# Kernel optimization log

Measured on AMD Instinct MI355X. Metric: run time of the kernel, lower is better.

The kernel has to match this reference:

```python
import jax, jax.numpy as jnp
import numpy as np

EPS = 1e-10


def setup_inputs() -> dict:
    key = jax.random.key(0)
    k1, k2, k3 = jax.random.split(key, 3)
    B, T, N = 32, 512, 128
    transition = jax.random.uniform(k1, (N, N), dtype=jnp.float32)
    log_emission = jax.random.normal(k2, (B, T, N), dtype=jnp.float32)
    prior = jax.random.uniform(k3, (N,), dtype=jnp.float32)
    return {"transition": transition, "log_emission": log_emission, "prior": prior}


def reference(transition, log_emission, prior):
    B, T, N = log_emission.shape
    # clamp + row-normalize transition (matches torch: clamp, clamp/sum(dim=1))
    trans = jnp.clip(transition, EPS)
    trans = jnp.clip(trans, EPS) / jnp.sum(trans, axis=1, keepdims=True)
    log_trans_T = jnp.log(trans).T  # (N, N): [next, prev]

    pr = jnp.clip(prior, EPS)
    pr = pr / jnp.sum(pr)
    log_prior = jnp.log(pr)

    # initial trellis row
    log0 = log_prior[None, :] + log_emission[:, 0]  # (B, N)
    em_rest = jnp.transpose(log_emission[:, 1:], (1, 0, 2))  # (T-1, B, N)

    def fwd_step(prev_log, em_t):
        # scores[b, next, prev] = prev_log[b, prev] + log_trans_T[next, prev]
        scores = prev_log[:, None, :] + log_trans_T[None, :, :]  # (B, N, N)
        m = jnp.max(scores, axis=-1, keepdims=True)
        e = jnp.exp(scores - m)
        Z = jnp.sum(e, axis=-1, keepdims=True)
        soft_max = jnp.squeeze(jnp.log(Z) + m, -1)  # logsumexp, (B, N)
        new_log = em_t + soft_max
        bp = e / Z  # soft backpointers, (B, N, N)
        return new_log, bp

    last_log, bps = jax.lax.scan(fwd_step, log0, em_rest)  # bps: (T-1, B, N, N)

    final_probs = jax.nn.softmax(last_log, axis=1)  # (B, N)

    def bwd_step(p_next, bp_t):
        # soft_path[t] = soft_path[t+1] @ bp[t]
        p = jnp.einsum("bn,bnm->bm", p_next, bp_t)
        return p, p

    _, path_prefix = jax.lax.scan(bwd_step, final_probs, bps, reverse=True)  # (T-1, B, N)

    soft_path = jnp.concatenate([path_prefix, final_probs[None]], axis=0)  # (T, B, N)
    return jnp.transpose(soft_path, (1, 0, 2))  # (B, T, N)
```

## Files before the change

### kernel.cpp

```cpp
#include <hip/hip_runtime.h>
#include <math.h>


#define TT 512
#define BB 32
#define NN 128
#define EPSC 1e-10f
#define TINY 1e-33f

#define BAR() asm volatile("s_waitcnt lgkmcnt(0)\n\ts_barrier" ::: "memory")

__device__ __forceinline__ float qswap1(float x) {
  return __int_as_float(__builtin_amdgcn_mov_dpp(__float_as_int(x), 0xB1, 0xF, 0xF, true));
}
__device__ __forceinline__ float qswap2(float x) {
  return __int_as_float(__builtin_amdgcn_mov_dpp(__float_as_int(x), 0x4E, 0xF, 0xF, true));
}

__device__ __forceinline__ void dot32(const float4 av[8], const float tm[2][32], float z[2]) {
  #pragma unroll
  for (int s = 0; s < 2; ++s) {
    float a0 = 0.f, a1 = 0.f, a2 = 0.f, a3 = 0.f;
    #pragma unroll
    for (int i = 0; i < 8; ++i) {
      a0 = fmaf(av[i].x, tm[s][4*i+0], a0);
      a1 = fmaf(av[i].y, tm[s][4*i+1], a1);
      a2 = fmaf(av[i].z, tm[s][4*i+2], a2);
      a3 = fmaf(av[i].w, tm[s][4*i+3], a3);
    }
    float zz = (a0 + a1) + (a2 + a3);
    zz += qswap1(zz);
    zz += qswap2(zz);
    z[s] = zz;
  }
}

__global__ __launch_bounds__(256, 1)
void soft_viterbi_kernel(const float* __restrict__ trans,
                         const float* __restrict__ emis,
                         const float* __restrict__ prior,
                         float* __restrict__ out) {
  const int b    = blockIdx.x;
  const int tid  = threadIdx.x;
  const int w    = tid >> 6;
  const int lane = tid & 63;
  const int k    = lane & 3;
  const int pid  = lane >> 2;
  const int n0   = 32 * w + 2 * pid;

  __shared__ __align__(16) float ubuf[2][NN];
  __shared__ __align__(16) float sarr[TT];
  __shared__ __align__(16) float red[NN];

  const float* embq = emis + (size_t)b * TT * NN + n0;
  float* outb = out + (size_t)b * TT * NN;

  float2 pr2 = *(const float2*)(prior + n0);
  float2 em0 = *(const float2*)(embq);
  float2 e1  = *(const float2*)(embq + 1 * NN);
  float2 e2  = *(const float2*)(embq + 2 * NN);
  float2 e3  = *(const float2*)(embq + 3 * NN);
  pr2.x = fmaxf(pr2.x, EPSC); pr2.y = fmaxf(pr2.y, EPSC);

  if (tid < NN) {
    const float4* row = (const float4*)(trans + tid * NN);
    float s = 0.f;
    #pragma unroll 8
    for (int j = 0; j < NN / 4; ++j) {
      float4 v = row[j];
      s += fmaxf(v.x, EPSC) + fmaxf(v.y, EPSC) + fmaxf(v.z, EPSC) + fmaxf(v.w, EPSC);
    }
    red[tid] = s;
  }
  __syncthreads();

  float tf[2][32];
  #pragma unroll
  for (int i = 0; i < 8; ++i) {
    #pragma unroll
    for (int c = 0; c < 4; ++c) {
      const int p = 4 * (k + 4 * i) + c;
      const float2 tv = *(const float2*)(trans + p * NN + n0);
      const float rp = red[p];
      tf[0][4*i+c] = fmaxf(tv.x, EPSC) / rp;
      tf[1][4*i+c] = fmaxf(tv.y, EPSC) / rp;
    }
  }
  float tb[2][32];
  #pragma unroll
  for (int s = 0; s < 2; ++s) {
    const float inv = 1.0f / red[n0 + s];
    const float4* rr = (const float4*)(trans + (n0 + s) * NN);
    #pragma unroll
    for (int i = 0; i < 8; ++i) {
      const float4 tv = rr[k + 4 * i];
      tb[s][4*i+0] = fmaxf(tv.x, EPSC) * inv;
      tb[s][4*i+1] = fmaxf(tv.y, EPSC) * inv;
      tb[s][4*i+2] = fmaxf(tv.z, EPSC) * inv;
      tb[s][4*i+3] = fmaxf(tv.w, EPSC) * inv;
    }
  }

  float vv = (k == 0) ? (pr2.x + pr2.y) : 0.f;
  #pragma unroll
  for (int m = 1; m < 64; m <<= 1) vv += __shfl_xor(vv, m, 64);
  __syncthreads();
  if (lane == 0) red[w] = vv;
  __syncthreads();
  const float psum = (red[0] + red[1]) + (red[2] + red[3]);

  float an0 = (pr2.x / psum) * __expf(em0.x);
  float an1 = (pr2.y / psum) * __expf(em0.y);
  if (k == 0) {
    float2 a2 = make_float2(an0, an1);
    *(float2*)&ubuf[0][n0] = a2;
    *(float2*)(outb + n0) = a2;
  }
  float dc0 = __expf(e1.x), dc1 = __expf(e1.y);
  float2 eh1 = e2;
  float2 eh2 = e3;
  float dl0 = dc0, dl1 = dc1;
  BAR();

  for (int t = 1; t < TT; ++t) {
    const float* rb = ubuf[(t - 1) & 1];
    const float r0 = rb[0];
    const float4* rb4 = (const float4*)rb;
    float4 av[8];
    #pragma unroll
    for (int i = 0; i < 8; ++i) av[i] = rb4[k + 4 * i];
    float z[2];
    dot32(av, tf, z);
    const float rinv = 1.0f / r0;
    dl0 = dc0; dl1 = dc1;
    an0 = (dc0 * rinv) * z[0];
    an1 = (dc1 * rinv) * z[1];
    dc0 = __expf(eh1.x); dc1 = __expf(eh1.y);
    eh1 = eh2;
    const int tpre = (t + 3 < TT) ? (t + 3) : (TT - 1);
    eh2 = *(const float2*)(embq + (size_t)tpre * NN);
    if (k == 0) {
      float2 a2 = make_float2(an0, an1);
      *(float2*)&ubuf[t & 1][n0] = a2;
      if (t < TT - 1) *(float2*)(outb + (size_t)t * NN + n0) = a2;
    }
    if (tid == 0) sarr[t - 1] = rinv;
    BAR();
  }

  float v2 = (k == 0) ? (an0 + an1) : 0.f;
  #pragma unroll
  for (int m = 1; m < 64; m <<= 1) v2 += __shfl_xor(v2, m, 64);
  if (lane == 0) red[w] = v2;
  __syncthreads();
  const float total = (red[0] + red[1]) + (red[2] + red[3]);
  const float itot = 1.0f / total;
  float pc0 = an0 * itot, pc1 = an1 * itot;
  if (k == 0) *(float2*)(outb + (size_t)(TT - 1) * NN + n0) = make_float2(pc0, pc1);

  asm volatile("s_waitcnt vmcnt(0)" ::: "memory");

  float2 ec_cur = *(const float2*)(outb + (size_t)(TT - 2) * NN + n0);
  float2 ec_h   = *(const float2*)(outb + (size_t)(TT - 3) * NN + n0);
  float2 em_b1  = *(const float2*)(embq + (size_t)(TT - 2) * NN);
  float2 em_b2  = *(const float2*)(embq + (size_t)(TT - 3) * NN);
  const float sl = sarr[TT - 2];
  float g0 = dl0 * sl / fmaxf(an0, TINY);
  float g1 = dl1 * sl / fmaxf(an1, TINY);

  for (int t = TT - 2; t >= 0; --t) {
    if (k == 0) {
      *(float2*)&ubuf[t & 1][n0] = make_float2(pc0 * g0, pc1 * g1);
    }
    const float sr = sarr[(t > 0) ? (t - 1) : 0];
    const float gn0 = __expf(em_b1.x) * sr / fmaxf(ec_cur.x, TINY);
    const float gn1 = __expf(em_b1.y) * sr / fmaxf(ec_cur.y, TINY);
    em_b1 = em_b2;
    const int tp = (t >= 2) ? (t - 2) : 0;
    em_b2 = *(const float2*)(embq + (size_t)tp * NN);
    BAR();
    const float4* qb4 = (const float4*)ubuf[t & 1];
    float4 av[8];
    #pragma unroll
    for (int i = 0; i < 8; ++i) av[i] = qb4[k + 4 * i];
    float z[2];
    dot32(av, tb, z);
    pc0 = ec_cur.x * z[0];
    pc1 = ec_cur.y * z[1];
    if (k == 0) *(float2*)(outb + (size_t)t * NN + n0) = make_float2(pc0, pc1);
    g0 = gn0; g1 = gn1;
    ec_cur = ec_h;
    ec_h = *(const float2*)(outb + (size_t)tp * NN + n0);
  }
}

extern "C" void kernel_launch(void* const* d_in, const int* in_sizes, int n_in,
                              void* d_out, int out_size, void* d_ws, size_t ws_size,
                              hipStream_t stream) {
  (void)in_sizes; (void)n_in; (void)d_ws; (void)ws_size; (void)out_size;
  const float* trans = (const float*)d_in[0];
  const float* emis  = (const float*)d_in[1];
  const float* prior = (const float*)d_in[2];
  float* out = (float*)d_out;
  soft_viterbi_kernel<<<dim3(BB), dim3(256), 0, stream>>>(trans, emis, prior, out);
}
```

Before: 452.3 us.

## Collapse per-batch block to a single wavefront, removing barriers from recurrence

Each batch sequence now runs on one 64-lane wavefront instead of four. The forward and backward recurrences can then drop s_barrier entirely and use a single LDS buffer with only compiler fences. Each lane now computes 8 output dot products with packed float2 FMAs and selects its two outputs after DPP reductions. Division is also replaced by hardware reciprocal. The cost is 4x more FLOPs per lane, very heavy register use (two 128-float transition tiles), and possible LDS ordering hazards that now rely on in-wave execution order.

Measured after the change: 901.0 us. +99.2%, slower.

```diff
diff --git a/kernel.cpp b/kernel.cpp
--- a/kernel.cpp
+++ b/kernel.cpp
@@ -8,8 +8,13 @@
 #define EPSC 1e-10f
 #define TINY 1e-33f
 
-#define BAR() asm volatile("s_waitcnt lgkmcnt(0)\n\ts_barrier" ::: "memory")
-
+typedef float v2f __attribute__((ext_vector_type(2)));
+
+#define CFENCE() asm volatile("" ::: "memory")
+
+__device__ __forceinline__ float rcp_fast(float x) {
+  return __builtin_amdgcn_rcpf(x);
+}
 __device__ __forceinline__ float qswap1(float x) {
   return __int_as_float(__builtin_amdgcn_mov_dpp(__float_as_int(x), 0xB1, 0xF, 0xF, true));
 }
@@ -17,180 +22,187 @@
   return __int_as_float(__builtin_amdgcn_mov_dpp(__float_as_int(x), 0x4E, 0xF, 0xF, true));
 }
 
-__device__ __forceinline__ void dot32(const float4 av[8], const float tm[2][32], float z[2]) {
-  #pragma unroll
-  for (int s = 0; s < 2; ++s) {
-    float a0 = 0.f, a1 = 0.f, a2 = 0.f, a3 = 0.f;
-    #pragma unroll
-    for (int i = 0; i < 8; ++i) {
-      a0 = fmaf(av[i].x, tm[s][4*i+0], a0);
-      a1 = fmaf(av[i].y, tm[s][4*i+1], a1);
-      a2 = fmaf(av[i].z, tm[s][4*i+2], a2);
-      a3 = fmaf(av[i].w, tm[s][4*i+3], a3);
-    }
-    float zz = (a0 + a1) + (a2 + a3);
-    zz += qswap1(zz);
-    zz += qswap2(zz);
-    z[s] = zz;
-  }
-}
-
-__global__ __launch_bounds__(256, 1)
+__device__ __forceinline__ float dot16pk(const v2f* av, const v2f* tm) {
+  v2f a0 = av[0] * tm[0];
+  v2f a1 = av[1] * tm[1];
+  #pragma unroll
+  for (int j = 2; j < 16; j += 2) {
+    a0 = __builtin_elementwise_fma(av[j+0], tm[j+0], a0);
+    a1 = __builtin_elementwise_fma(av[j+1], tm[j+1], a1);
+  }
+  v2f s = a0 + a1;
+  return s.x + s.y;
+}
+
+__global__ __launch_bounds__(64, 1)
 void soft_viterbi_kernel(const float* __restrict__ trans,
                          const float* __restrict__ emis,
                          const float* __restrict__ prior,
                          float* __restrict__ out) {
   const int b    = blockIdx.x;
-  const int tid  = threadIdx.x;
-  const int w    = tid >> 6;
-  const int lane = tid & 63;
+  const int lane = threadIdx.x;
+  const int g    = lane >> 2;
   const int k    = lane & 3;
-  const int pid  = lane >> 2;
-  const int n0   = 32 * w + 2 * pid;
-
-  __shared__ __align__(16) float ubuf[2][NN];
+  const int s0   = 8 * g + 2 * k;
+  const int nf0  = 8 * g;
+  const bool k1  = (k & 1) != 0;
+  const bool k2  = (k & 2) != 0;
+
+  __shared__ __align__(16) float ubuf[NN];
   __shared__ __align__(16) float sarr[TT];
   __shared__ __align__(16) float red[NN];
 
-  const float* embq = emis + (size_t)b * TT * NN + n0;
-  float* outb = out + (size_t)b * TT * NN;
-
-  float2 pr2 = *(const float2*)(prior + n0);
-  float2 em0 = *(const float2*)(embq);
-  float2 e1  = *(const float2*)(embq + 1 * NN);
-  float2 e2  = *(const float2*)(embq + 2 * NN);
-  float2 e3  = *(const float2*)(embq + 3 * NN);
+  const float* emB = emis + (size_t)b * TT * NN;
+  float* outb      = out  + (size_t)b * TT * NN;
+
+  float2 pr2 = *(const float2*)(prior + s0);
+  float2 em0 = *(const float2*)(emB + s0);
+  float2 e1  = *(const float2*)(emB + 1 * NN + s0);
+  float2 e2  = *(const float2*)(emB + 2 * NN + s0);
+  float2 e3  = *(const float2*)(emB + 3 * NN + s0);
   pr2.x = fmaxf(pr2.x, EPSC); pr2.y = fmaxf(pr2.y, EPSC);
 
-  if (tid < NN) {
-    const float4* row = (const float4*)(trans + tid * NN);
+  #pragma unroll
+  for (int rr = 0; rr < 2; ++rr) {
+    const int r = 2 * lane + rr;
+    const float4* row = (const float4*)(trans + r * NN);
     float s = 0.f;
     #pragma unroll 8
     for (int j = 0; j < NN / 4; ++j) {
       float4 v = row[j];
       s += fmaxf(v.x, EPSC) + fmaxf(v.y, EPSC) + fmaxf(v.z, EPSC) + fmaxf(v.w, EPSC);
     }
-    red[tid] = s;
-  }
-  __syncthreads();
-
-  float tf[2][32];
+    red[r] = s;
+  }
+  CFENCE();
+
+  v2f tf[8][16];
   #pragma unroll
   for (int i = 0; i < 8; ++i) {
     #pragma unroll
     for (int c = 0; c < 4; ++c) {
       const int p = 4 * (k + 4 * i) + c;
-      const float2 tv = *(const float2*)(trans + p * NN + n0);
-      const float rp = red[p];
-      tf[0][4*i+c] = fmaxf(tv.x, EPSC) / rp;
-      tf[1][4*i+c] = fmaxf(tv.y, EPSC) / rp;
+      const float4 ta = *(const float4*)(trans + p * NN + nf0);
+      const float4 tc = *(const float4*)(trans + p * NN + nf0 + 4);
+      const float ir = 1.0f / red[p];
+      const int jj = 2 * i + (c >> 1); const int ee = c & 1;
+      tf[0][jj][ee] = fmaxf(ta.x, EPSC) * ir;
+      tf[1][jj][ee] = fmaxf(ta.y, EPSC) * ir;
+      tf[2][jj][ee] = fmaxf(ta.z, EPSC) * ir;
+      tf[3][jj][ee] = fmaxf(ta.w, EPSC) * ir;
+      tf[4][jj][ee] = fmaxf(tc.x, EPSC) * ir;
+      tf[5][jj][ee] = fmaxf(tc.y, EPSC) * ir;
+      tf[6][jj][ee] = fmaxf(tc.z, EPSC) * ir;
+      tf[7][jj][ee] = fmaxf(tc.w, EPSC) * ir;
     }
   }
-  float tb[2][32];
-  #pragma unroll
-  for (int s = 0; s < 2; ++s) {
-    const float inv = 1.0f / red[n0 + s];
-    const float4* rr = (const float4*)(trans + (n0 + s) * NN);
-    #pragma unroll
-    for (int i = 0; i < 8; ++i) {
-      const float4 tv = rr[k + 4 * i];
-      tb[s][4*i+0] = fmaxf(tv.x, EPSC) * inv;
-      tb[s][4*i+1] = fmaxf(tv.y, EPSC) * inv;
-      tb[s][4*i+2] = fmaxf(tv.z, EPSC) * inv;
-      tb[s][4*i+3] = fmaxf(tv.w, EPSC) * inv;
-    }
-  }
-
-  float vv = (k == 0) ? (pr2.x + pr2.y) : 0.f;
+
+  float vv = pr2.x + pr2.y;
   #pragma unroll
   for (int m = 1; m < 64; m <<= 1) vv += __shfl_xor(vv, m, 64);
-  __syncthreads();
-  if (lane == 0) red[w] = vv;
-  __syncthreads();
-  const float psum = (red[0] + red[1]) + (red[2] + red[3]);
+  const float psum = vv;
 
   float an0 = (pr2.x / psum) * __expf(em0.x);
   float an1 = (pr2.y / psum) * __expf(em0.y);
-  if (k == 0) {
-    float2 a2 = make_float2(an0, an1);
-    *(float2*)&ubuf[0][n0] = a2;
-    *(float2*)(outb + n0) = a2;
-  }
+  *(float2*)&ubuf[s0] = make_float2(an0, an1);
+  *(float2*)(outb + s0) = make_float2(an0, an1);
+  float rinv = rcp_fast(__int_as_float(__builtin_amdgcn_readfirstlane(__float_as_int(an0))));
+  if (lane == 0) sarr[0] = rinv;
   float dc0 = __expf(e1.x), dc1 = __expf(e1.y);
   float2 eh1 = e2;
   float2 eh2 = e3;
-  float dl0 = dc0, dl1 = dc1;
-  BAR();
 
   for (int t = 1; t < TT; ++t) {
-    const float* rb = ubuf[(t - 1) & 1];
-    const float r0 = rb[0];
-    const float4* rb4 = (const float4*)rb;
-    float4 av[8];
-    #pragma unroll
-    for (int i = 0; i < 8; ++i) av[i] = rb4[k + 4 * i];
-    float z[2];
-    dot32(av, tf, z);
-    const float rinv = 1.0f / r0;
-    dl0 = dc0; dl1 = dc1;
-    an0 = (dc0 * rinv) * z[0];
-    an1 = (dc1 * rinv) * z[1];
-    dc0 = __expf(eh1.x); dc1 = __expf(eh1.y);
+    CFENCE();
+    float4 a4[8];
+    #pragma unroll
+    for (int i = 0; i < 8; ++i) a4[i] = *(const float4*)&ubuf[4 * (k + 4 * i)];
+    const float ndc0 = __expf(eh1.x), ndc1 = __expf(eh1.y);
     eh1 = eh2;
     const int tpre = (t + 3 < TT) ? (t + 3) : (TT - 1);
-    eh2 = *(const float2*)(embq + (size_t)tpre * NN);
-    if (k == 0) {
-      float2 a2 = make_float2(an0, an1);
-      *(float2*)&ubuf[t & 1][n0] = a2;
-      if (t < TT - 1) *(float2*)(outb + (size_t)t * NN + n0) = a2;
+    eh2 = *(const float2*)(emB + (size_t)tpre * NN + s0);
+    const v2f* av = (const v2f*)a4;
+    float z[8];
+    #pragma unroll
+    for (int s = 0; s < 8; ++s) z[s] = dot16pk(av, tf[s]);
+    #pragma unroll
+    for (int s = 0; s < 8; ++s) { z[s] += qswap1(z[s]); z[s] += qswap2(z[s]); }
+    const float zl0 = k1 ? z[2] : z[0], zl1 = k1 ? z[3] : z[1];
+    const float zh0 = k1 ? z[6] : z[4], zh1 = k1 ? z[7] : z[5];
+    const float za = k2 ? zh0 : zl0;
+    const float zb = k2 ? zh1 : zl1;
+    an0 = (dc0 * rinv) * za;
+    an1 = (dc1 * rinv) * zb;
+    *(float2*)&ubuf[s0] = make_float2(an0, an1);
+    if (t < TT - 1) *(float2*)(outb + (size_t)t * NN + s0) = make_float2(an0, an1);
+    rinv = rcp_fast(__int_as_float(__builtin_amdgcn_readfirstlane(__float_as_int(an0))));
+    if (lane == 0) sarr[t] = rinv;
+    dc0 = ndc0; dc1 = ndc1;
+  }
+  const float dl0 = dc0, dl1 = dc1;
+
+  float v2 = an0 + an1;
+  #pragma unroll
+  for (int m = 1; m < 64; m <<= 1) v2 += __shfl_xor(v2, m, 64);
+  const float itot = 1.0f / v2;
+  float pc0 = an0 * itot, pc1 = an1 * itot;
+  *(float2*)(outb + (size_t)(TT - 1) * NN + s0) = make_float2(pc0, pc1);
+
+  asm volatile("s_waitcnt vmcnt(0)" ::: "memory");
+
+  v2f tb[8][16];
+  #pragma unroll
+  for (int s = 0; s < 8; ++s) {
+    const float ir = 1.0f / red[nf0 + s];
+    const float4* rr = (const float4*)(trans + (nf0 + s) * NN);
+    #pragma unroll
+    for (int i = 0; i < 8; ++i) {
+      const float4 tv = rr[k + 4 * i];
+      tb[s][2*i+0][0] = fmaxf(tv.x, EPSC) * ir;
+      tb[s][2*i+0][1] = fmaxf(tv.y, EPSC) * ir;
+      tb[s][2*i+1][0] = fmaxf(tv.z, EPSC) * ir;
+      tb[s][2*i+1][1] = fmaxf(tv.w, EPSC) * ir;
     }
-    if (tid == 0) sarr[t - 1] = rinv;
-    BAR();
-  }
-
-  float v2 = (k == 0) ? (an0 + an1) : 0.f;
-  #pragma unroll
-  for (int m = 1; m < 64; m <<= 1) v2 += __shfl_xor(v2, m, 64);
-  if (lane == 0) red[w] = v2;
-  __syncthreads();
-  const float total = (red[0] + red[1]) + (red[2] + red[3]);
-  const float itot = 1.0f / total;
-  float pc0 = an0 * itot, pc1 = an1 * itot;
-  if (k == 0) *(float2*)(outb + (size_t)(TT - 1) * NN + n0) = make_float2(pc0, pc1);
-
-  asm volatile("s_waitcnt vmcnt(0)" ::: "memory");
-
-  float2 ec_cur = *(const float2*)(outb + (size_t)(TT - 2) * NN + n0);
-  float2 ec_h   = *(const float2*)(outb + (size_t)(TT - 3) * NN + n0);
-  float2 em_b1  = *(const float2*)(embq + (size_t)(TT - 2) * NN);
-  float2 em_b2  = *(const float2*)(embq + (size_t)(TT - 3) * NN);
+  }
+
+  float2 ec_cur = *(const float2*)(outb + (size_t)(TT - 2) * NN + s0);
+  float2 ec_h   = *(const float2*)(outb + (size_t)(TT - 3) * NN + s0);
+  float2 em_b1  = *(const float2*)(emB  + (size_t)(TT - 2) * NN + s0);
+  float2 em_b2  = *(const float2*)(emB  + (size_t)(TT - 3) * NN + s0);
   const float sl = sarr[TT - 2];
-  float g0 = dl0 * sl / fmaxf(an0, TINY);
-  float g1 = dl1 * sl / fmaxf(an1, TINY);
+  float g0 = dl0 * sl * rcp_fast(fmaxf(an0, TINY));
+  float g1 = dl1 * sl * rcp_fast(fmaxf(an1, TINY));
 
   for (int t = TT - 2; t >= 0; --t) {
-    if (k == 0) {
-      *(float2*)&ubuf[t & 1][n0] = make_float2(pc0 * g0, pc1 * g1);
-    }
+    CFENCE();
+    *(float2*)&ubuf[s0] = make_float2(pc0 * g0, pc1 * g1);
+    CFENCE();
+    float4 a4[8];
+    #pragma unroll
+    for (int i = 0; i < 8; ++i) a4[i] = *(const float4*)&ubuf[4 * (k + 4 * i)];
     const float sr = sarr[(t > 0) ? (t - 1) : 0];
-    const float gn0 = __expf(em_b1.x) * sr / fmaxf(ec_cur.x, TINY);
-    const float gn1 = __expf(em_b1.y) * sr / fmaxf(ec_cur.y, TINY);
+    const float at0 = ec_cur.x, at1 = ec_cur.y;
+    const float gn0 = __expf(em_b1.x) * sr * rcp_fast(fmaxf(at0, TINY));
+    const float gn1 = __expf(em_b1.y) * sr * rcp_fast(fmaxf(at1, TINY));
     em_b1 = em_b2;
     const int tp = (t >= 2) ? (t - 2) : 0;
-    em_b2 = *(const float2*)(embq + (size_t)tp * NN);
-    BAR();
-    const float4* qb4 = (const float4*)ubuf[t & 1];
-    float4 av[8];
-    #pragma unroll
-    for (int i = 0; i < 8; ++i) av[i] = qb4[k + 4 * i];
-    float z[2];
-    dot32(av, tb, z);
-    pc0 = ec_cur.x * z[0];
-    pc1 = ec_cur.y * z[1];
-    if (k == 0) *(float2*)(outb + (size_t)t * NN + n0) = make_float2(pc0, pc1);
+    em_b2 = *(const float2*)(emB + (size_t)tp * NN + s0);
+    const v2f* av = (const v2f*)a4;
+    float z[8];
+    #pragma unroll
+    for (int s = 0; s < 8; ++s) z[s] = dot16pk(av, tb[s]);
+    #pragma unroll
+    for (int s = 0; s < 8; ++s) { z[s] += qswap1(z[s]); z[s] += qswap2(z[s]); }
+    const float zl0 = k1 ? z[2] : z[0], zl1 = k1 ? z[3] : z[1];
+    const float zh0 = k1 ? z[6] : z[4], zh1 = k1 ? z[7] : z[5];
+    const float za = k2 ? zh0 : zl0;
+    const float zb = k2 ? zh1 : zl1;
+    pc0 = at0 * za;
+    pc1 = at1 * zb;
+    *(float2*)(outb + (size_t)t * NN + s0) = make_float2(pc0, pc1);
     g0 = gn0; g1 = gn1;
     ec_cur = ec_h;
-    ec_h = *(const float2*)(outb + (size_t)tp * NN + n0);
+    ec_h = *(const float2*)(outb + (size_t)tp * NN + s0);
   }
 }
 
@@ -202,5 +214,5 @@
   const float* emis  = (const float*)d_in[1];
   const float* prior = (const float*)d_in[2];
   float* out = (float*)d_out;
-  soft_viterbi_kernel<<<dim3(BB), dim3(256), 0, stream>>>(trans, emis, prior, out);
-}
+  soft_viterbi_kernel<<<dim3(BB), dim3(64), 0, stream>>>(trans, emis, prior, out);
+}
```
